# Kernel tuning notes

Hardware: AMD Instinct MI355X
Metric: run time of the kernel (lower is better)

The kernel has to match this reference:

```python
import jax, jax.numpy as jnp
import numpy as np

De, Dv = 128, 128


def _layernorm(x, g, b, eps=1e-5):
    m = jnp.mean(x, axis=-1, keepdims=True)
    v = jnp.var(x, axis=-1, keepdims=True)
    return (x - m) * jax.lax.rsqrt(v + eps) * g + b


def _gelu(x):
    return jax.nn.gelu(x, approximate=False)


def setup_inputs() -> dict:
    key = jax.random.key(0)
    ks = jax.random.split(key, 20)
    Z, N, Kn = 4, 2048, 30
    inp = {
        'V_new': jax.random.normal(ks[0], (Z, N, Dv), jnp.float32),
        'V_old': jax.random.normal(ks[1], (Z, N, Dv), jnp.float32),
        'E': jax.random.normal(ks[2], (Z, N, Kn, De), jnp.float32),
        'S': jax.random.normal(ks[3], (Z, N, De), jnp.float32),
        'K_idx': jax.random.randint(ks[4], (Z, N, Kn), 0, N, jnp.int32),
        'edge_mask': jax.random.bernoulli(ks[5], 0.9, (Z, N, Kn)),
        'autoregressive_mask': jax.random.bernoulli(ks[6], 0.5, (Z, N, Kn)),
    }
    d_in = 2 * De + 2 * Dv  # 512
    s = lambda fan_in: 1.0 / np.sqrt(fan_in)
    # node_messenger MLP: in->Dv, gelu, Dv->Dv, gelu, Dv->Dv (hidden_layers=1)
    inp['W_m0'] = jax.random.uniform(ks[7], (d_in, Dv), jnp.float32, -s(d_in), s(d_in))
    inp['b_m0'] = jnp.zeros((Dv,), jnp.float32)
    inp['W_m1'] = jax.random.uniform(ks[8], (Dv, Dv), jnp.float32, -s(Dv), s(Dv))
    inp['b_m1'] = jnp.zeros((Dv,), jnp.float32)
    inp['W_m2'] = jax.random.uniform(ks[9], (Dv, Dv), jnp.float32, -s(Dv), s(Dv))
    inp['b_m2'] = jnp.zeros((Dv,), jnp.float32)
    inp['g_mn'] = jnp.ones((Dv,), jnp.float32)
    inp['beta_mn'] = jnp.zeros((Dv,), jnp.float32)
    # ffn MLP: Dv->4Dv, gelu, 4Dv->Dv (hidden_layers=0)
    inp['W_f0'] = jax.random.uniform(ks[10], (Dv, 4 * Dv), jnp.float32, -s(Dv), s(Dv))
    inp['b_f0'] = jnp.zeros((4 * Dv,), jnp.float32)
    inp['W_f1'] = jax.random.uniform(ks[11], (4 * Dv, Dv), jnp.float32, -s(4 * Dv), s(4 * Dv))
    inp['b_f1'] = jnp.zeros((Dv,), jnp.float32)
    inp['g_fn'] = jnp.ones((Dv,), jnp.float32)
    inp['beta_fn'] = jnp.zeros((Dv,), jnp.float32)
    return inp


def reference(V_new, V_old, E, S, K_idx, edge_mask, autoregressive_mask,
              W_m0, b_m0, W_m1, b_m1, W_m2, b_m2, g_mn, beta_mn,
              W_f0, b_f0, W_f1, b_f1, g_fn, beta_fn):
    Z, N, Kn = K_idx.shape
    zidx = jnp.arange(Z)[:, None, None]
    Es = jnp.where(autoregressive_mask[..., None], S[zidx, K_idx], 0.0)  # [Z,N,K,De]
    Ecat = jnp.concatenate([E, Es], axis=3)  # [Z,N,K,2*De]
    # gather_nodes
    Vi = jnp.broadcast_to(V_new[:, :, None, :], (Z, N, Kn, Dv))
    Vj_new = V_new[zidx, K_idx]  # [Z,N,K,Dv]
    Vj_old = V_old[zidx, K_idx]
    Vj = jnp.where(autoregressive_mask[..., None], Vj_new, Vj_old)
    Mv_pre = jnp.concatenate([Vi, Vj, Ecat], axis=3)  # [Z,N,K,2Dv+2De]
    # node_messenger MLP (pointwise)
    h = _gelu(Mv_pre @ W_m0 + b_m0)
    h = _gelu(h @ W_m1 + b_m1)
    Mv = h @ W_m2 + b_m2
    Mv = jnp.where(edge_mask[..., None], Mv, 0.0)
    V = _layernorm(V_new + Mv.sum(axis=2), g_mn, beta_mn)
    ffn = _gelu(V @ W_f0 + b_f0) @ W_f1 + b_f1
    V = _layernorm(V + ffn, g_fn, beta_fn)
    return V
```

## Files before the change

kernel.cpp:

```cpp
#include <hip/hip_runtime.h>
#include <math.h>

#define NN 2048
#define KN 30

typedef __bf16 bf16x8 __attribute__((ext_vector_type(8)));
typedef float f32x4 __attribute__((ext_vector_type(4)));
typedef unsigned short u16x8 __attribute__((ext_vector_type(8)));
typedef unsigned short u16x4 __attribute__((ext_vector_type(4)));

__device__ __forceinline__ unsigned short f2bf(float f) {
  unsigned u = __builtin_bit_cast(unsigned, f);
  u += 0x7FFFu + ((u >> 16) & 1u);
  return (unsigned short)(u >> 16);
}

__device__ __forceinline__ float gelu_f(float x) {
  return 0.5f * x * (1.0f + erff(x * 0.70710678118654752f));
}

__device__ __forceinline__ bool rdmask(const void* p, int i, int mode) {
  if (mode == 1) return ((const unsigned char*)p)[i] != 0;
  if (mode == 2) return ((const float*)p)[i] != 0.0f;
  return ((const int*)p)[i] != 0;
}

__device__ __forceinline__ bf16x8 ld_afrag(const char* base, int row, int rowstride, int s, int g) {
  int byte = row * rowstride + s * 64 + g * 16;
  byte ^= (row & 7) << 4;
  u16x8 u = *(const u16x8*)(base + byte);
  return __builtin_bit_cast(bf16x8, u);
}

__device__ __forceinline__ bf16x8 ld_bfrag(const u16x8* __restrict__ pw, int s, int t, int NT, int lane) {
  u16x8 u = pw[(s * NT + t) * 64 + lane];
  return __builtin_bit_cast(bf16x8, u);
}

__global__ void k0_pack(const float* __restrict__ Wm0, const float* __restrict__ Wm1,
                        const float* __restrict__ Wm2, const float* __restrict__ Wf0,
                        const float* __restrict__ Wf1, unsigned short* __restrict__ dst) {
  int i = blockIdx.x * 256 + threadIdx.x;
  if (i >= 229376) return;
  const float* W;
  int base, Nc;
  if (i < 65536)       { W = Wm0; base = 0;      Nc = 128; }
  else if (i < 81920)  { W = Wm1; base = 65536;  Nc = 128; }
  else if (i < 98304)  { W = Wm2; base = 81920;  Nc = 128; }
  else if (i < 163840) { W = Wf0; base = 98304;  Nc = 512; }
  else                 { W = Wf1; base = 163840; Nc = 128; }
  int NT = Nc >> 4;
  int p = i - base;
  int j = p & 7;
  int l = (p >> 3) & 63;
  int rest = p >> 9;
  int t = rest % NT;
  int s = rest / NT;
  int kk = 32 * s + 8 * (l >> 4) + j;
  int c = 16 * t + (l & 15);
  dst[i] = f2bf(W[kk * Nc + c]);
}

__global__ __launch_bounds__(256, 3) void k1_edge_mlp(
    const float* __restrict__ Vnew, const float* __restrict__ Vold,
    const float* __restrict__ E, const float* __restrict__ S,
    const int* __restrict__ Kidx, const void* __restrict__ emask,
    const void* __restrict__ amask,
    const float* __restrict__ Wm0f,
    const u16x8* __restrict__ pWm0, const u16x8* __restrict__ pWm1,
    const u16x8* __restrict__ pWm2,
    const float* __restrict__ bm0, const float* __restrict__ bm1,
    const float* __restrict__ bm2,
    float* __restrict__ Msum) {
  extern __shared__ char smem[];
  float* vb = (float*)(smem + 49152);
  float* em_lds = (float*)(smem + 50176);
  unsigned long long* ptrs = (unsigned long long*)(smem + 50432);
  const int tid = threadIdx.x;
  const int p = blockIdx.x;
  const int z = (2 * p) / NN;
  const int n0 = (2 * p) % NN;

  if (tid < 64) {
    int boff = (z * NN + n0) * KN;
    if (boff > 245760 - 256) boff = 245760 - 256;
    unsigned dv = *(const unsigned*)((const char*)emask + boff + 4 * tid);
    unsigned long long b1 = __ballot(dv == 1u);
    unsigned long long bf = __ballot(dv == 0x3F800000u);
    int mode = (__popcll(bf) > 16) ? 2 : ((__popcll(b1) > 16) ? 0 : 1);
    int row = tid;
    const float *pVj = nullptr, *pE = nullptr, *pEs = nullptr;
    float em = 0.f;
    if (row < 60) {
      int ln = row >= 30;
      int n = n0 + ln;
      int k = row - 30 * ln;
      int eidx = (z * NN + n) * KN + k;
      int kidx = Kidx[eidx];
      bool am = rdmask(amask, eidx, mode);
      em = rdmask(emask, eidx, mode) ? 1.0f : 0.0f;
      pVj = (am ? Vnew : Vold) + (z * NN + kidx) * 128;
      pE = E + (long)eidx * 128;
      pEs = am ? (S + (z * NN + kidx) * 128) : nullptr;
    }
    em_lds[row] = em;
    ptrs[row * 3 + 0] = (unsigned long long)pVj;
    ptrs[row * 3 + 1] = (unsigned long long)pE;
    ptrs[row * 3 + 2] = (unsigned long long)pEs;
  }

  {
    int nd = tid >> 7, col = tid & 127;
    const float* vi = Vnew + (z * NN + n0 + nd) * 128;
    float a0 = 0.f, a1 = 0.f, a2 = 0.f, a3 = 0.f;
#pragma unroll 8
    for (int k = 0; k < 128; k += 4) {
      a0 = fmaf(vi[k + 0], Wm0f[(k + 0) * 128 + col], a0);
      a1 = fmaf(vi[k + 1], Wm0f[(k + 1) * 128 + col], a1);
      a2 = fmaf(vi[k + 2], Wm0f[(k + 2) * 128 + col], a2);
      a3 = fmaf(vi[k + 3], Wm0f[(k + 3) * 128 + col], a3);
    }
    vb[nd * 128 + col] = (a0 + a1) + (a2 + a3);
  }
  __syncthreads();

#pragma unroll 4
  for (int i = 0; i < 12; ++i) {
    int pf = i * 256 + tid;
    int t = pf >> 4;
    int row = (t * 2731) >> 13;
    int rem = pf - row * 48;
    int seg = rem >> 4;
    int idx2 = rem & 15;
    const float4* sp = (const float4*)ptrs[row * 3 + seg];
    float4 v0 = sp ? sp[2 * idx2] : make_float4(0.f, 0.f, 0.f, 0.f);
    float4 v1 = sp ? sp[2 * idx2 + 1] : make_float4(0.f, 0.f, 0.f, 0.f);
    u16x8 h;
    h[0] = f2bf(v0.x); h[1] = f2bf(v0.y); h[2] = f2bf(v0.z); h[3] = f2bf(v0.w);
    h[4] = f2bf(v1.x); h[5] = f2bf(v1.y); h[6] = f2bf(v1.z); h[7] = f2bf(v1.w);
    int byte = row * 768 + ((seg * 256 + idx2 * 16) ^ ((row & 7) << 4));
    *(u16x8*)(smem + byte) = h;
  }
  __syncthreads();

  const int w = tid >> 6, l = tid & 63;
  const int r = l & 15, g = l >> 4;
  float bb0[2], bb1[2], bb2[2];
#pragma unroll
  for (int tt = 0; tt < 2; ++tt) {
    int col = 32 * w + 16 * tt + r;
    bb0[tt] = bm0[col]; bb1[tt] = bm1[col]; bb2[tt] = bm2[col];
  }
  const f32x4 zf = {0.f, 0.f, 0.f, 0.f};

  f32x4 acc[4][2];
#pragma unroll
  for (int mt = 0; mt < 4; ++mt)
#pragma unroll
    for (int tt = 0; tt < 2; ++tt) acc[mt][tt] = zf;
  for (int s = 0; s < 12; ++s) {
    bf16x8 a[4];
#pragma unroll
    for (int mt = 0; mt < 4; ++mt) a[mt] = ld_afrag(smem, 16 * mt + r, 768, s, g);
#pragma unroll
    for (int tt = 0; tt < 2; ++tt) {
      bf16x8 b = ld_bfrag(pWm0, s + 4, 2 * w + tt, 8, l);
#pragma unroll
      for (int mt = 0; mt < 4; ++mt)
        acc[mt][tt] = __builtin_amdgcn_mfma_f32_16x16x32_bf16(a[mt], b, acc[mt][tt], 0, 0, 0);
    }
  }
  __syncthreads();
  char* h0 = smem;
#pragma unroll
  for (int mt = 0; mt < 4; ++mt)
#pragma unroll
    for (int tt = 0; tt < 2; ++tt)
#pragma unroll
      for (int j = 0; j < 4; ++j) {
        int row = 16 * mt + 4 * g + j;
        int col = 32 * w + 16 * tt + r;
        float v = 0.f;
        if (row < 60)
          v = gelu_f(acc[mt][tt][j] + vb[(row >= 30) * 128 + col] + bb0[tt]);
        int byte = row * 256 + col * 2;
        byte ^= (row & 7) << 4;
        *(unsigned short*)(h0 + byte) = f2bf(v);
      }
  __syncthreads();

  char* h1 = smem + 16384;
  {
    f32x4 acc1[4][2];
#pragma unroll
    for (int mt = 0; mt < 4; ++mt)
#pragma unroll
      for (int tt = 0; tt < 2; ++tt) acc1[mt][tt] = zf;
#pragma unroll
    for (int s = 0; s < 4; ++s) {
      bf16x8 a[4];
#pragma unroll
      for (int mt = 0; mt < 4; ++mt) a[mt] = ld_afrag(h0, 16 * mt + r, 256, s, g);
#pragma unroll
      for (int tt = 0; tt < 2; ++tt) {
        bf16x8 b = ld_bfrag(pWm1, s, 2 * w + tt, 8, l);
#pragma unroll
        for (int mt = 0; mt < 4; ++mt)
          acc1[mt][tt] = __builtin_amdgcn_mfma_f32_16x16x32_bf16(a[mt], b, acc1[mt][tt], 0, 0, 0);
      }
    }
#pragma unroll
    for (int mt = 0; mt < 4; ++mt)
#pragma unroll
      for (int tt = 0; tt < 2; ++tt)
#pragma unroll
        for (int j = 0; j < 4; ++j) {
          int row = 16 * mt + 4 * g + j;
          int col = 32 * w + 16 * tt + r;
          float v = gelu_f(acc1[mt][tt][j] + bb1[tt]);
          int byte = row * 256 + col * 2;
          byte ^= (row & 7) << 4;
          *(unsigned short*)(h1 + byte) = f2bf(v);
        }
  }
  __syncthreads();

  {
    f32x4 acc2[4][2];
#pragma unroll
    for (int mt = 0; mt < 4; ++mt)
#pragma unroll
      for (int tt = 0; tt < 2; ++tt) acc2[mt][tt] = zf;
#pragma unroll
    for (int s = 0; s < 4; ++s) {
      bf16x8 a[4];
#pragma unroll
      for (int mt = 0; mt < 4; ++mt) a[mt] = ld_afrag(h1, 16 * mt + r, 256, s, g);
#pragma unroll
      for (int tt = 0; tt < 2; ++tt) {
        bf16x8 b = ld_bfrag(pWm2, s, 2 * w + tt, 8, l);
#pragma unroll
        for (int mt = 0; mt < 4; ++mt)
          acc2[mt][tt] = __builtin_amdgcn_mfma_f32_16x16x32_bf16(a[mt], b, acc2[mt][tt], 0, 0, 0);
      }
    }
    float s0[2] = {0.f, 0.f}, s1[2] = {0.f, 0.f};
#pragma unroll
    for (int mt = 0; mt < 4; ++mt)
#pragma unroll
      for (int tt = 0; tt < 2; ++tt)
#pragma unroll
        for (int j = 0; j < 4; ++j) {
          int row = 16 * mt + 4 * g + j;
          float v = (acc2[mt][tt][j] + bb2[tt]) * em_lds[row];
          if (row < 30) s0[tt] += v; else s1[tt] += v;
        }
#pragma unroll
    for (int tt = 0; tt < 2; ++tt) {
      s0[tt] += __shfl_xor(s0[tt], 16); s0[tt] += __shfl_xor(s0[tt], 32);
      s1[tt] += __shfl_xor(s1[tt], 16); s1[tt] += __shfl_xor(s1[tt], 32);
    }
    if (g == 0) {
#pragma unroll
      for (int tt = 0; tt < 2; ++tt)
        Msum[(z * NN + n0) * 128 + 32 * w + 16 * tt + r] = s0[tt];
    } else if (g == 1) {
#pragma unroll
      for (int tt = 0; tt < 2; ++tt)
        Msum[(z * NN + n0 + 1) * 128 + 32 * w + 16 * tt + r] = s1[tt];
    }
  }
}

__global__ __launch_bounds__(256, 2) void k2_ffn(
    const float* __restrict__ Vnew, const float* __restrict__ Msum,
    const u16x8* __restrict__ pWf0, const u16x8* __restrict__ pWf1,
    const float* __restrict__ bf0, const float* __restrict__ bf1,
    const float* __restrict__ gmn, const float* __restrict__ bmn,
    const float* __restrict__ gfn, const float* __restrict__ bfn,
    float* __restrict__ out) {
  extern __shared__ char smem[];
  float* V1f = (float*)smem;
  char* A1 = smem + 8192;
  char* hb = smem + 12288;
  const int tid = threadIdx.x;
  const int g0 = blockIdx.x * 16;

  {
    int rr = tid >> 4, sub = tid & 15;
    int rowflat = g0 + rr;
    const float4* vn = (const float4*)(Vnew + rowflat * 128 + sub * 8);
    const float4* ms = (const float4*)(Msum + rowflat * 128 + sub * 8);
    float4 a0 = vn[0], a1 = vn[1], m0 = ms[0], m1 = ms[1];
    float v[8] = {a0.x + m0.x, a0.y + m0.y, a0.z + m0.z, a0.w + m0.w,
                  a1.x + m1.x, a1.y + m1.y, a1.z + m1.z, a1.w + m1.w};
    float s = 0.f, sq = 0.f;
#pragma unroll
    for (int i = 0; i < 8; ++i) { s += v[i]; sq += v[i] * v[i]; }
    s += __shfl_xor(s, 1);  sq += __shfl_xor(sq, 1);
    s += __shfl_xor(s, 2);  sq += __shfl_xor(sq, 2);
    s += __shfl_xor(s, 4);  sq += __shfl_xor(sq, 4);
    s += __shfl_xor(s, 8);  sq += __shfl_xor(sq, 8);
    float mean = s * (1.0f / 128.0f);
    float var = sq * (1.0f / 128.0f) - mean * mean;
    float inv = rsqrtf(var + 1e-5f);
    u16x4 h0v, h1v;
#pragma unroll
    for (int i = 0; i < 8; ++i) {
      int c = sub * 8 + i;
      float x = (v[i] - mean) * inv * gmn[c] + bmn[c];
      V1f[rr * 128 + c] = x;
      if (i < 4) h0v[i] = f2bf(x); else h1v[i - 4] = f2bf(x);
    }
    int byte = rr * 256 + ((sub * 16) ^ ((rr & 7) << 4));
    *(u16x4*)(A1 + byte) = h0v;
    *(u16x4*)(A1 + byte + 8) = h1v;
  }
  __syncthreads();

  const int w = tid >> 6, l = tid & 63;
  const int r = l & 15, g = l >> 4;
  const f32x4 zf = {0.f, 0.f, 0.f, 0.f};

  {
    f32x4 acc[8];
#pragma unroll
    for (int tt = 0; tt < 8; ++tt) acc[tt] = zf;
#pragma unroll
    for (int s = 0; s < 4; ++s) {
      bf16x8 a = ld_afrag(A1, r, 256, s, g);
#pragma unroll
      for (int tt = 0; tt < 8; ++tt) {
        bf16x8 b = ld_bfrag(pWf0, s, 8 * w + tt, 32, l);
        acc[tt] = __builtin_amdgcn_mfma_f32_16x16x32_bf16(a, b, acc[tt], 0, 0, 0);
      }
    }
#pragma unroll
    for (int tt = 0; tt < 8; ++tt) {
      int col = 128 * w + 16 * tt + r;
      float bias = bf0[col];
#pragma unroll
      for (int j = 0; j < 4; ++j) {
        int row = 4 * g + j;
        float v = gelu_f(acc[tt][j] + bias);
        int byte = row * 1024 + col * 2;
        byte ^= (row & 7) << 4;
        *(unsigned short*)(hb + byte) = f2bf(v);
      }
    }
  }
  __syncthreads();

  {
    f32x4 acc2[2];
#pragma unroll
    for (int tt = 0; tt < 2; ++tt) acc2[tt] = zf;
    for (int s = 0; s < 16; ++s) {
      bf16x8 a = ld_afrag(hb, r, 1024, s, g);
#pragma unroll
      for (int tt = 0; tt < 2; ++tt) {
        bf16x8 b = ld_bfrag(pWf1, s, 2 * w + tt, 8, l);
        acc2[tt] = __builtin_amdgcn_mfma_f32_16x16x32_bf16(a, b, acc2[tt], 0, 0, 0);
      }
    }
    __syncthreads();
    float* op = (float*)(smem + 8192);
#pragma unroll
    for (int tt = 0; tt < 2; ++tt)
#pragma unroll
      for (int j = 0; j < 4; ++j) {
        int row = 4 * g + j;
        int col = 32 * w + 16 * tt + r;
        op[row * 128 + col] = V1f[row * 128 + col] + acc2[tt][j] + bf1[col];
      }
  }
  __syncthreads();

  {
    const float* op = (const float*)(smem + 8192);
    int rr = tid >> 4, sub = tid & 15;
    float v[8];
    float s = 0.f, sq = 0.f;
#pragma unroll
    for (int i = 0; i < 8; ++i) {
      v[i] = op[rr * 128 + sub * 8 + i];
      s += v[i]; sq += v[i] * v[i];
    }
    s += __shfl_xor(s, 1);  sq += __shfl_xor(sq, 1);
    s += __shfl_xor(s, 2);  sq += __shfl_xor(sq, 2);
    s += __shfl_xor(s, 4);  sq += __shfl_xor(sq, 4);
    s += __shfl_xor(s, 8);  sq += __shfl_xor(sq, 8);
    float mean = s * (1.0f / 128.0f);
    float var = sq * (1.0f / 128.0f) - mean * mean;
    float inv = rsqrtf(var + 1e-5f);
    int rowflat = g0 + rr;
    float* dst = out + rowflat * 128 + sub * 8;
    float4 o0, o1;
    int c = sub * 8;
    o0.x = (v[0] - mean) * inv * gfn[c + 0] + bfn[c + 0];
    o0.y = (v[1] - mean) * inv * gfn[c + 1] + bfn[c + 1];
    o0.z = (v[2] - mean) * inv * gfn[c + 2] + bfn[c + 2];
    o0.w = (v[3] - mean) * inv * gfn[c + 3] + bfn[c + 3];
    o1.x = (v[4] - mean) * inv * gfn[c + 4] + bfn[c + 4];
    o1.y = (v[5] - mean) * inv * gfn[c + 5] + bfn[c + 5];
    o1.z = (v[6] - mean) * inv * gfn[c + 6] + bfn[c + 6];
    o1.w = (v[7] - mean) * inv * gfn[c + 7] + bfn[c + 7];
    ((float4*)dst)[0] = o0;
    ((float4*)dst)[1] = o1;
  }
}

extern "C" void kernel_launch(void* const* d_in, const int* in_sizes, int n_in,
                              void* d_out, int out_size, void* d_ws, size_t ws_size,
                              hipStream_t stream) {
  const float* Vnew = (const float*)d_in[0];
  const float* Vold = (const float*)d_in[1];
  const float* E    = (const float*)d_in[2];
  const float* S    = (const float*)d_in[3];
  const int* Kidx   = (const int*)d_in[4];
  const void* emask = d_in[5];
  const void* amask = d_in[6];
  const float* Wm0 = (const float*)d_in[7];  const float* bm0 = (const float*)d_in[8];
  const float* Wm1 = (const float*)d_in[9];  const float* bm1 = (const float*)d_in[10];
  const float* Wm2 = (const float*)d_in[11]; const float* bm2 = (const float*)d_in[12];
  const float* gmn = (const float*)d_in[13]; const float* bmn = (const float*)d_in[14];
  const float* Wf0 = (const float*)d_in[15]; const float* bf0 = (const float*)d_in[16];
  const float* Wf1 = (const float*)d_in[17]; const float* bf1 = (const float*)d_in[18];
  const float* gfn = (const float*)d_in[19]; const float* bfn = (const float*)d_in[20];

  unsigned short* pack = (unsigned short*)d_ws;
  float* Msum = (float*)((char*)d_ws + 458752);
  float* out = (float*)d_out;

  k0_pack<<<896, 256, 0, stream>>>(Wm0, Wm1, Wm2, Wf0, Wf1, pack);
  k1_edge_mlp<<<4096, 256, 51968, stream>>>(
      Vnew, Vold, E, S, Kidx, emask, amask, Wm0,
      (const u16x8*)pack, (const u16x8*)(pack + 65536), (const u16x8*)(pack + 81920),
      bm0, bm1, bm2, Msum);
  k2_ffn<<<512, 256, 28672, stream>>>(
      Vnew, Msum,
      (const u16x8*)(pack + 98304), (const u16x8*)(pack + 163840),
      bf0, bf1, gmn, bmn, gfn, bfn, out);
}
```

Baseline: 360.5 us.

## Process one node per edge-MLP block and precompute Vi projection separately

The edge MLP kernel now handles one node (30 edges, padded to 32 rows) per block instead of two, which halves LDS use and register tiles so the launch bound can target 6 blocks per CU. The Vi @ W_m0 projection is moved into a separate kernel that writes a workspace buffer, used when the workspace is large enough, with a fallback that computes it in-block. Per-block MFMA tiles shrink, so B-fragment weight loads are amortised over fewer rows, and there is an extra launch plus a global round trip for the projection.

```diff
diff --git a/kernel.cpp b/kernel.cpp
--- a/kernel.cpp
+++ b/kernel.cpp
@@ -61,57 +61,73 @@
   dst[i] = f2bf(W[kk * Nc + c]);
 }
 
-__global__ __launch_bounds__(256, 3) void k1_edge_mlp(
+__global__ __launch_bounds__(256) void kvb(const float* __restrict__ Vnew,
+                                           const float* __restrict__ Wm0f,
+                                           float* __restrict__ VB) {
+  int col = threadIdx.x & 127, half = threadIdx.x >> 7;
+  int base = blockIdx.x * 16 + half * 8;
+  float acc[8] = {0.f, 0.f, 0.f, 0.f, 0.f, 0.f, 0.f, 0.f};
+#pragma unroll 4
+  for (int k = 0; k < 128; ++k) {
+    float wv = Wm0f[k * 128 + col];
+#pragma unroll
+    for (int r = 0; r < 8; ++r)
+      acc[r] = fmaf(Vnew[(base + r) * 128 + k], wv, acc[r]);
+  }
+#pragma unroll
+  for (int r = 0; r < 8; ++r) VB[(base + r) * 128 + col] = acc[r];
+}
+
+template <bool UV>
+__global__ __launch_bounds__(256, 6) void k1_edge_mlp(
     const float* __restrict__ Vnew, const float* __restrict__ Vold,
     const float* __restrict__ E, const float* __restrict__ S,
     const int* __restrict__ Kidx, const void* __restrict__ emask,
     const void* __restrict__ amask,
-    const float* __restrict__ Wm0f,
+    const float* __restrict__ VB, const float* __restrict__ Wm0f,
     const u16x8* __restrict__ pWm0, const u16x8* __restrict__ pWm1,
     const u16x8* __restrict__ pWm2,
     const float* __restrict__ bm0, const float* __restrict__ bm1,
     const float* __restrict__ bm2,
     float* __restrict__ Msum) {
   extern __shared__ char smem[];
-  float* vb = (float*)(smem + 49152);
-  float* em_lds = (float*)(smem + 50176);
-  unsigned long long* ptrs = (unsigned long long*)(smem + 50432);
+  float* vb = (float*)(smem + 24576);
+  float* em_lds = (float*)(smem + 25088);
+  unsigned long long* ptrs = (unsigned long long*)(smem + 25216);
   const int tid = threadIdx.x;
   const int p = blockIdx.x;
-  const int z = (2 * p) / NN;
-  const int n0 = (2 * p) % NN;
+  const int z = p >> 11;
+  const int n = p & (NN - 1);
 
   if (tid < 64) {
-    int boff = (z * NN + n0) * KN;
-    if (boff > 245760 - 256) boff = 245760 - 256;
-    unsigned dv = *(const unsigned*)((const char*)emask + boff + 4 * tid);
+    unsigned dv = *(const unsigned*)((const char*)emask + 4 * tid);
     unsigned long long b1 = __ballot(dv == 1u);
-    unsigned long long bf = __ballot(dv == 0x3F800000u);
-    int mode = (__popcll(bf) > 16) ? 2 : ((__popcll(b1) > 16) ? 0 : 1);
+    unsigned long long bfp = __ballot(dv == 0x3F800000u);
+    int mode = (__popcll(bfp) > 16) ? 2 : ((__popcll(b1) > 16) ? 0 : 1);
     int row = tid;
-    const float *pVj = nullptr, *pE = nullptr, *pEs = nullptr;
-    float em = 0.f;
-    if (row < 60) {
-      int ln = row >= 30;
-      int n = n0 + ln;
-      int k = row - 30 * ln;
-      int eidx = (z * NN + n) * KN + k;
-      int kidx = Kidx[eidx];
-      bool am = rdmask(amask, eidx, mode);
-      em = rdmask(emask, eidx, mode) ? 1.0f : 0.0f;
-      pVj = (am ? Vnew : Vold) + (z * NN + kidx) * 128;
-      pE = E + (long)eidx * 128;
-      pEs = am ? (S + (z * NN + kidx) * 128) : nullptr;
-    }
-    em_lds[row] = em;
-    ptrs[row * 3 + 0] = (unsigned long long)pVj;
-    ptrs[row * 3 + 1] = (unsigned long long)pE;
-    ptrs[row * 3 + 2] = (unsigned long long)pEs;
-  }
-
-  {
-    int nd = tid >> 7, col = tid & 127;
-    const float* vi = Vnew + (z * NN + n0 + nd) * 128;
+    if (row < 32) {
+      const float *pVj = nullptr, *pE = nullptr, *pEs = nullptr;
+      float em = 0.f;
+      if (row < 30) {
+        int eidx = (z * NN + n) * KN + row;
+        int kidx = Kidx[eidx];
+        bool am = rdmask(amask, eidx, mode);
+        em = rdmask(emask, eidx, mode) ? 1.0f : 0.0f;
+        pVj = (am ? Vnew : Vold) + (z * NN + kidx) * 128;
+        pE = E + (long)eidx * 128;
+        pEs = am ? (S + (z * NN + kidx) * 128) : nullptr;
+      }
+      em_lds[row] = em;
+      ptrs[row * 3 + 0] = (unsigned long long)pVj;
+      ptrs[row * 3 + 1] = (unsigned long long)pE;
+      ptrs[row * 3 + 2] = (unsigned long long)pEs;
+    }
+  }
+  if (UV) {
+    if (tid >= 64 && tid < 192) vb[tid - 64] = VB[(z * NN + n) * 128 + (tid - 64)];
+  } else if (tid >= 128) {
+    int col = tid - 128;
+    const float* vi = Vnew + (z * NN + n) * 128;
     float a0 = 0.f, a1 = 0.f, a2 = 0.f, a3 = 0.f;
 #pragma unroll 8
     for (int k = 0; k < 128; k += 4) {
@@ -120,12 +136,12 @@
       a2 = fmaf(vi[k + 2], Wm0f[(k + 2) * 128 + col], a2);
       a3 = fmaf(vi[k + 3], Wm0f[(k + 3) * 128 + col], a3);
     }
-    vb[nd * 128 + col] = (a0 + a1) + (a2 + a3);
-  }
-  __syncthreads();
-
-#pragma unroll 4
-  for (int i = 0; i < 12; ++i) {
+    vb[col] = (a0 + a1) + (a2 + a3);
+  }
+  __syncthreads();
+
+#pragma unroll
+  for (int i = 0; i < 6; ++i) {
     int pf = i * 256 + tid;
     int t = pf >> 4;
     int row = (t * 2731) >> 13;
@@ -153,27 +169,27 @@
   }
   const f32x4 zf = {0.f, 0.f, 0.f, 0.f};
 
-  f32x4 acc[4][2];
-#pragma unroll
-  for (int mt = 0; mt < 4; ++mt)
+  f32x4 acc[2][2];
+#pragma unroll
+  for (int mt = 0; mt < 2; ++mt)
 #pragma unroll
     for (int tt = 0; tt < 2; ++tt) acc[mt][tt] = zf;
   for (int s = 0; s < 12; ++s) {
-    bf16x8 a[4];
-#pragma unroll
-    for (int mt = 0; mt < 4; ++mt) a[mt] = ld_afrag(smem, 16 * mt + r, 768, s, g);
+    bf16x8 a[2];
+#pragma unroll
+    for (int mt = 0; mt < 2; ++mt) a[mt] = ld_afrag(smem, 16 * mt + r, 768, s, g);
 #pragma unroll
     for (int tt = 0; tt < 2; ++tt) {
       bf16x8 b = ld_bfrag(pWm0, s + 4, 2 * w + tt, 8, l);
 #pragma unroll
-      for (int mt = 0; mt < 4; ++mt)
+      for (int mt = 0; mt < 2; ++mt)
         acc[mt][tt] = __builtin_amdgcn_mfma_f32_16x16x32_bf16(a[mt], b, acc[mt][tt], 0, 0, 0);
     }
   }
   __syncthreads();
   char* h0 = smem;
 #pragma unroll
-  for (int mt = 0; mt < 4; ++mt)
+  for (int mt = 0; mt < 2; ++mt)
 #pragma unroll
     for (int tt = 0; tt < 2; ++tt)
 #pragma unroll
@@ -181,36 +197,36 @@
         int row = 16 * mt + 4 * g + j;
         int col = 32 * w + 16 * tt + r;
         float v = 0.f;
-        if (row < 60)
-          v = gelu_f(acc[mt][tt][j] + vb[(row >= 30) * 128 + col] + bb0[tt]);
+        if (row < 30)
+          v = gelu_f(acc[mt][tt][j] + vb[col] + bb0[tt]);
         int byte = row * 256 + col * 2;
         byte ^= (row & 7) << 4;
         *(unsigned short*)(h0 + byte) = f2bf(v);
       }
   __syncthreads();
 
-  char* h1 = smem + 16384;
-  {
-    f32x4 acc1[4][2];
-#pragma unroll
-    for (int mt = 0; mt < 4; ++mt)
+  char* h1 = smem + 8192;
+  {
+    f32x4 acc1[2][2];
+#pragma unroll
+    for (int mt = 0; mt < 2; ++mt)
 #pragma unroll
       for (int tt = 0; tt < 2; ++tt) acc1[mt][tt] = zf;
 #pragma unroll
     for (int s = 0; s < 4; ++s) {
-      bf16x8 a[4];
-#pragma unroll
-      for (int mt = 0; mt < 4; ++mt) a[mt] = ld_afrag(h0, 16 * mt + r, 256, s, g);
+      bf16x8 a[2];
+#pragma unroll
+      for (int mt = 0; mt < 2; ++mt) a[mt] = ld_afrag(h0, 16 * mt + r, 256, s, g);
 #pragma unroll
       for (int tt = 0; tt < 2; ++tt) {
         bf16x8 b = ld_bfrag(pWm1, s, 2 * w + tt, 8, l);
 #pragma unroll
-        for (int mt = 0; mt < 4; ++mt)
+        for (int mt = 0; mt < 2; ++mt)
           acc1[mt][tt] = __builtin_amdgcn_mfma_f32_16x16x32_bf16(a[mt], b, acc1[mt][tt], 0, 0, 0);
       }
     }
 #pragma unroll
-    for (int mt = 0; mt < 4; ++mt)
+    for (int mt = 0; mt < 2; ++mt)
 #pragma unroll
       for (int tt = 0; tt < 2; ++tt)
 #pragma unroll
@@ -226,48 +242,43 @@
   __syncthreads();
 
   {
-    f32x4 acc2[4][2];
-#pragma unroll
-    for (int mt = 0; mt < 4; ++mt)
+    f32x4 acc2[2][2];
+#pragma unroll
+    for (int mt = 0; mt < 2; ++mt)
 #pragma unroll
       for (int tt = 0; tt < 2; ++tt) acc2[mt][tt] = zf;
 #pragma unroll
     for (int s = 0; s < 4; ++s) {
-      bf16x8 a[4];
-#pragma unroll
-      for (int mt = 0; mt < 4; ++mt) a[mt] = ld_afrag(h1, 16 * mt + r, 256, s, g);
+      bf16x8 a[2];
+#pragma unroll
+      for (int mt = 0; mt < 2; ++mt) a[mt] = ld_afrag(h1, 16 * mt + r, 256, s, g);
 #pragma unroll
       for (int tt = 0; tt < 2; ++tt) {
         bf16x8 b = ld_bfrag(pWm2, s, 2 * w + tt, 8, l);
 #pragma unroll
-        for (int mt = 0; mt < 4; ++mt)
+        for (int mt = 0; mt < 2; ++mt)
           acc2[mt][tt] = __builtin_amdgcn_mfma_f32_16x16x32_bf16(a[mt], b, acc2[mt][tt], 0, 0, 0);
       }
     }
-    float s0[2] = {0.f, 0.f}, s1[2] = {0.f, 0.f};
-#pragma unroll
-    for (int mt = 0; mt < 4; ++mt)
+    float s0[2] = {0.f, 0.f};
+#pragma unroll
+    for (int mt = 0; mt < 2; ++mt)
 #pragma unroll
       for (int tt = 0; tt < 2; ++tt)
 #pragma unroll
         for (int j = 0; j < 4; ++j) {
           int row = 16 * mt + 4 * g + j;
-          float v = (acc2[mt][tt][j] + bb2[tt]) * em_lds[row];
-          if (row < 30) s0[tt] += v; else s1[tt] += v;
+          s0[tt] += (acc2[mt][tt][j] + bb2[tt]) * em_lds[row];
         }
 #pragma unroll
     for (int tt = 0; tt < 2; ++tt) {
-      s0[tt] += __shfl_xor(s0[tt], 16); s0[tt] += __shfl_xor(s0[tt], 32);
-      s1[tt] += __shfl_xor(s1[tt], 16); s1[tt] += __shfl_xor(s1[tt], 32);
+      s0[tt] += __shfl_xor(s0[tt], 16);
+      s0[tt] += __shfl_xor(s0[tt], 32);
     }
     if (g == 0) {
 #pragma unroll
       for (int tt = 0; tt < 2; ++tt)
-        Msum[(z * NN + n0) * 128 + 32 * w + 16 * tt + r] = s0[tt];
-    } else if (g == 1) {
-#pragma unroll
-      for (int tt = 0; tt < 2; ++tt)
-        Msum[(z * NN + n0 + 1) * 128 + 32 * w + 16 * tt + r] = s1[tt];
+        Msum[(z * NN + n) * 128 + 32 * w + 16 * tt + r] = s0[tt];
     }
   }
 }
@@ -429,14 +440,26 @@
   const float* gfn = (const float*)d_in[19]; const float* bfn = (const float*)d_in[20];
 
   unsigned short* pack = (unsigned short*)d_ws;
-  float* Msum = (float*)((char*)d_ws + 458752);
+  const size_t need = 458752u + 4194304u + 4194304u;
+  bool useVB = ws_size >= need;
+  float* VB = (float*)((char*)d_ws + 458752);
+  float* Msum = useVB ? (float*)((char*)d_ws + 458752 + 4194304)
+                      : (float*)((char*)d_ws + 458752);
   float* out = (float*)d_out;
 
   k0_pack<<<896, 256, 0, stream>>>(Wm0, Wm1, Wm2, Wf0, Wf1, pack);
-  k1_edge_mlp<<<4096, 256, 51968, stream>>>(
-      Vnew, Vold, E, S, Kidx, emask, amask, Wm0,
-      (const u16x8*)pack, (const u16x8*)(pack + 65536), (const u16x8*)(pack + 81920),
-      bm0, bm1, bm2, Msum);
+  if (useVB) {
+    kvb<<<512, 256, 0, stream>>>(Vnew, Wm0, VB);
+    k1_edge_mlp<true><<<8192, 256, 25984, stream>>>(
+        Vnew, Vold, E, S, Kidx, emask, amask, VB, Wm0,
+        (const u16x8*)pack, (const u16x8*)(pack + 65536), (const u16x8*)(pack + 81920),
+        bm0, bm1, bm2, Msum);
+  } else {
+    k1_edge_mlp<false><<<8192, 256, 25984, stream>>>(
+        Vnew, Vold, E, S, Kidx, emask, amask, VB, Wm0,
+        (const u16x8*)pack, (const u16x8*)(pack + 65536), (const u16x8*)(pack + 81920),
+        bm0, bm1, bm2, Msum);
+  }
   k2_ffn<<<512, 256, 28672, stream>>>(
       Vnew, Msum,
       (const u16x8*)(pack + 98304), (const u16x8*)(pack + 163840),
```

After: 336.2 us. -6.8%, faster.
